# Optimization experiments

Measured on AMD Instinct MI355X. Metric: run time of the kernel, lower is better.

The kernel has to match this reference:

```python
import jax, jax.numpy as jnp
import numpy as np

K = 4096          # num_embeddings
D = 256           # embedding_dim
COMMIT = 0.25     # commitment_cost


def setup_inputs() -> dict:
    key = jax.random.key(0)
    k1, k2 = jax.random.split(key)
    z = jax.random.normal(k1, (16, D, 32, 32), dtype=jnp.float32)
    # codebook init: uniform(-1/K, 1/K) as in the torch module
    emb = jax.random.uniform(k2, (K, D), dtype=jnp.float32,
                             minval=-1.0 / K, maxval=1.0 / K)
    return {"z": z, "emb": emb}


def reference(z, emb):
    B, Dm, H, W = z.shape
    # (B, D, H, W) -> (B*H*W, D)
    z_flat = jnp.transpose(z, (0, 2, 3, 1)).reshape(-1, Dm)
    # squared L2 distances to every codebook vector: (N, K)
    distances = (jnp.sum(z_flat * z_flat, axis=1, keepdims=True)
                 + jnp.sum(emb * emb, axis=1)
                 - 2.0 * jnp.matmul(z_flat, emb.T))
    encoding_indices = jnp.argmin(distances, axis=1)            # (N,)
    encodings = jax.nn.one_hot(encoding_indices, emb.shape[0],
                               dtype=z.dtype)                   # (N, K)
    quantized = jnp.take(emb, encoding_indices, axis=0)         # == encodings @ emb

    sg = jax.lax.stop_gradient
    e_latent_loss = jnp.mean((sg(quantized) - z_flat) ** 2)
    q_latent_loss = jnp.mean((quantized - sg(z_flat)) ** 2)
    loss = q_latent_loss + COMMIT * e_latent_loss

    avg_probs = jnp.mean(encodings, axis=0)
    perplexity = jnp.exp(-jnp.sum(avg_probs * jnp.log(avg_probs + 1e-10)))

    # straight-through estimator
    quantized = z_flat + sg(quantized - z_flat)
    # NOTE: faithful to source: torch does .view(B, D, H, W) on the (N, D)
    # flat tensor WITHOUT permuting back -- a plain reshape, replicated here.
    quantized = quantized.reshape(B, Dm, H, W)
    return quantized, loss, perplexity, encodings
```

## Files before the change

### kernel.cpp

```cpp
#include <hip/hip_runtime.h>

#define NN 16384
#define KK 4096
#define DD 256

typedef __attribute__((ext_vector_type(8))) short short8;
typedef __attribute__((ext_vector_type(4))) float f32x4;

static __device__ __forceinline__ unsigned short f2bf(float f) {
  unsigned u = __float_as_uint(f);
  return (unsigned short)((u + 0x7FFFu + ((u >> 16) & 1u)) >> 16);
}

static __device__ __forceinline__ unsigned int mono(float f) {
  unsigned u = __float_as_uint(f);
  return (u & 0x80000000u) ? ~u : (u | 0x80000000u);
}

__global__ __launch_bounds__(256) void vq_prep(
    const float* __restrict__ z, const float* __restrict__ emb,
    unsigned short* __restrict__ zb, unsigned short* __restrict__ eb,
    float* __restrict__ e2g, unsigned long long* __restrict__ keys,
    unsigned int* __restrict__ counts, float* __restrict__ lossacc,
    unsigned int* __restrict__ donecnt) {
  __shared__ unsigned short t[64][72];
  const int tid = threadIdx.x;
  const int bx = blockIdx.x;

  if (bx < 1024) {
    const int b = bx >> 6, rem = bx & 63, dt = rem >> 4, ht = rem & 15;
    const float* src = z + (long)b * 262144 + (long)dt * 65536 + ht * 64;
    #pragma unroll
    for (int p = 0; p < 16; ++p) {
      int idx = p * 256 + tid;
      int dl = idx >> 6, hl = idx & 63;
      t[hl][dl] = f2bf(src[dl * 1024 + hl]);
    }
    __syncthreads();
    unsigned short* dst = zb + ((long)b * 1024 + (long)ht * 64) * DD + dt * 64;
    #pragma unroll
    for (int p = 0; p < 2; ++p) {
      int idx = p * 256 + tid;
      int hl = idx >> 3, c8 = idx & 7;
      short8 v = *reinterpret_cast<const short8*>(&t[hl][c8 * 8]);
      *reinterpret_cast<short8*>(&dst[(long)hl * DD + c8 * 8]) = v;
    }
  } else if (bx < 2048) {
    const int wid = tid >> 6, lane = tid & 63;
    const int row = (bx - 1024) * 4 + wid;
    float4 v = *reinterpret_cast<const float4*>(&emb[row * DD + lane * 4]);
    ushort4 w;
    w.x = f2bf(v.x); w.y = f2bf(v.y); w.z = f2bf(v.z); w.w = f2bf(v.w);
    *reinterpret_cast<ushort4*>(&eb[row * DD + lane * 4]) = w;
    float s = v.x * v.x + v.y * v.y + v.z * v.z + v.w * v.w;
    #pragma unroll
    for (int o = 1; o < 64; o <<= 1) s += __shfl_xor(s, o);
    if (lane == 0) e2g[row] = s;
  } else {
    int tt = (bx - 2048) * 256 + tid;
    #pragma unroll
    for (int i = 0; i < 8; ++i) keys[tt * 8 + i] = ~0ull;
    counts[tt * 2] = 0u;
    counts[tt * 2 + 1] = 0u;
    if (tt == 0) { lossacc[0] = 0.f; donecnt[0] = 0u; }
  }
}

__global__ __launch_bounds__(256) void vq_gemm(
    const unsigned short* __restrict__ eb, const unsigned short* __restrict__ zb,
    const float* __restrict__ e2g, unsigned long long* __restrict__ keys,
    float* __restrict__ enc) {
  __shared__ unsigned short At[2][128 * 64];
  __shared__ unsigned short Bt[2][128 * 64];
  __shared__ float e2s[128];
  __shared__ unsigned long long wkey[2][128];

  const int tid = threadIdx.x;
  const int bm = blockIdx.x;
  const int bn = blockIdx.y;
  const int lane = tid & 63, wid = tid >> 6;
  const int wm = wid >> 1, wn = wid & 1;
  const int l16 = lane & 15, g4 = lane >> 4;

  if (tid < 128) {
    e2s[tid] = e2g[bm * 128 + tid];
    wkey[0][tid] = ~0ull;
    wkey[1][tid] = ~0ull;
  }

  const long abase = (long)bm * 128 * DD;
  const long bbase = (long)bn * 128 * DD;
  const int lr = lane >> 3, lc = (lane & 7) * 8;

  auto stage = [&](int buf, int kt) {
    #pragma unroll
    for (int c = 0; c < 4; ++c) {
      const int row0 = wid * 32 + c * 8;
      const unsigned short* ga =
          eb + abase + (long)(row0 + lr) * DD + kt * 64 + lc;
      __builtin_amdgcn_global_load_lds(
          (const __attribute__((address_space(1))) void*)ga,
          (__attribute__((address_space(3))) void*)&At[buf][row0 * 64], 16, 0, 0);
      const unsigned short* gb =
          zb + bbase + (long)(row0 + lr) * DD + kt * 64 + lc;
      __builtin_amdgcn_global_load_lds(
          (const __attribute__((address_space(1))) void*)gb,
          (__attribute__((address_space(3))) void*)&Bt[buf][row0 * 64], 16, 0, 0);
    }
  };

  f32x4 acc[4][4];
  #pragma unroll
  for (int mi = 0; mi < 4; ++mi)
    #pragma unroll
    for (int ni = 0; ni < 4; ++ni) acc[mi][ni] = (f32x4){0.f, 0.f, 0.f, 0.f};

  stage(0, 0);
  #pragma unroll
  for (int kt = 0; kt < 4; ++kt) {
    const int cur = kt & 1;
    asm volatile("s_waitcnt lgkmcnt(0)" ::: "memory");
    __builtin_amdgcn_s_barrier();
    if (kt < 3) {
      stage(cur ^ 1, kt + 1);
      asm volatile("s_waitcnt vmcnt(8)" ::: "memory");
    } else {
      asm volatile("s_waitcnt vmcnt(0)" ::: "memory");
    }
    __builtin_amdgcn_s_barrier();

    #pragma unroll
    for (int kk = 0; kk < 2; ++kk) {
      short8 a[4], b[4];
      #pragma unroll
      for (int mi = 0; mi < 4; ++mi)
        a[mi] = *reinterpret_cast<const short8*>(
            &At[cur][(wm * 64 + mi * 16 + l16) * 64 + kk * 32 + g4 * 8]);
      #pragma unroll
      for (int ni = 0; ni < 4; ++ni)
        b[ni] = *reinterpret_cast<const short8*>(
            &Bt[cur][(wn * 64 + ni * 16 + l16) * 64 + kk * 32 + g4 * 8]);
      #pragma unroll
      for (int mi = 0; mi < 4; ++mi)
        #pragma unroll
        for (int ni = 0; ni < 4; ++ni)
          acc[mi][ni] = __builtin_amdgcn_mfma_f32_16x16x32_bf16(
              a[mi], b[ni], acc[mi][ni], 0, 0, 0);
    }
  }

  #pragma unroll
  for (int ni = 0; ni < 4; ++ni) {
    float bv = INFINITY;
    int bi = 0;
    #pragma unroll
    for (int mi = 0; mi < 4; ++mi) {
      #pragma unroll
      for (int r = 0; r < 4; ++r) {
        int krow = wm * 64 + mi * 16 + g4 * 4 + r;
        float s = fmaf(-2.0f, acc[mi][ni][r], e2s[krow]);
        if (s < bv) { bv = s; bi = bm * 128 + krow; }
      }
    }
    unsigned long long key =
        ((unsigned long long)mono(bv) << 32) | (unsigned)bi;
    unsigned long long o;
    o = __shfl_xor(key, 16); if (o < key) key = o;
    o = __shfl_xor(key, 32); if (o < key) key = o;
    if (g4 == 0) wkey[wm][wn * 64 + ni * 16 + l16] = key;
  }
  __syncthreads();
  if (tid < 128) {
    unsigned long long k0 = wkey[0][tid], k1 = wkey[1][tid];
    atomicMin(&keys[(long)bn * 128 + tid], k0 < k1 ? k0 : k1);
  }

  {
    const long base = ((long)(bm * 128 + bn)) * 16384;
    const f32x4 zero4 = (f32x4){0.f, 0.f, 0.f, 0.f};
    #pragma unroll
    for (int i = 0; i < 16; ++i)
      *reinterpret_cast<f32x4*>(&enc[base + (long)(i * 256 + tid) * 4]) = zero4;
  }
}

__global__ __launch_bounds__(256) void vq_finish(
    const float* __restrict__ z, const float* __restrict__ emb,
    const unsigned long long* __restrict__ keys, unsigned int* __restrict__ counts,
    float* __restrict__ lossacc, unsigned int* __restrict__ donecnt,
    float* __restrict__ outq, float* __restrict__ enc, float* __restrict__ outs) {
  __shared__ float ztile[64][257];
  __shared__ int sidx[64];
  __shared__ float wsum[4];
  __shared__ double sh[256];
  __shared__ unsigned int lastflag;

  const int tid = threadIdx.x;
  const int n0 = blockIdx.x * 64;
  const long zbase = (long)(n0 >> 10) * 262144 + (long)(n0 & 1023);

  {
    int n4 = (tid & 15) << 2;
    int dl = tid >> 4;
    for (int p = 0; p < 16; ++p) {
      int d = p * 16 + dl;
      float4 v = *reinterpret_cast<const float4*>(&z[zbase + (long)d * 1024 + n4]);
      ztile[n4 + 0][d] = v.x;
      ztile[n4 + 1][d] = v.y;
      ztile[n4 + 2][d] = v.z;
      ztile[n4 + 3][d] = v.w;
    }
  }
  if (tid < 64) {
    int n = n0 + tid;
    int idx = (int)(keys[n] & 0xFFFFFFFFULL);
    sidx[tid] = idx;
    atomicAdd(&counts[idx], 1u);
    enc[(long)n * KK + idx] = 1.0f;
  }
  __syncthreads();

  float lacc = 0.f;
  const int d = tid;
  #pragma unroll 4
  for (int nl = 0; nl < 64; ++nl) {
    int idx = sidx[nl];
    float e = emb[idx * DD + d];
    float zz = ztile[nl][d];
    float df = e - zz;
    lacc += df * df;
    outq[(long)(n0 + nl) * DD + d] = zz + (e - zz);
  }
  #pragma unroll
  for (int o = 1; o < 64; o <<= 1) lacc += __shfl_xor(lacc, o);
  if ((tid & 63) == 0) wsum[tid >> 6] = lacc;
  __syncthreads();
  if (tid == 0) atomicAdd(lossacc, wsum[0] + wsum[1] + wsum[2] + wsum[3]);

  __threadfence();
  if (tid == 0) lastflag = (atomicAdd(donecnt, 1u) == (unsigned)(NN / 64 - 1));
  __syncthreads();
  if (lastflag) {
    double ent = 0.0;
    for (int k = tid; k < KK; k += 256) {
      unsigned c = atomicAdd(&counts[k], 0u);
      double p = (double)c / (double)NN;
      ent += p * log(p + 1e-10);
    }
    sh[tid] = ent;
    __syncthreads();
    for (int s = 128; s > 0; s >>= 1) {
      if (tid < s) sh[tid] += sh[tid + s];
      __syncthreads();
    }
    if (tid == 0) {
      float la = atomicAdd(lossacc, 0.f);
      outs[0] = la * 1.25f / ((float)NN * (float)DD);
      outs[1] = (float)exp(-sh[0]);
    }
  }
}

extern "C" void kernel_launch(void* const* d_in, const int* in_sizes, int n_in,
                              void* d_out, int out_size, void* d_ws, size_t ws_size,
                              hipStream_t stream) {
  const float* z = (const float*)d_in[0];
  const float* emb = (const float*)d_in[1];
  float* out = (float*)d_out;
  float* outq = out;
  float* outs = out + 4194304;
  float* enc = out + 4194306;

  char* ws = (char*)d_ws;
  unsigned short* zb = (unsigned short*)ws;
  unsigned short* eb = (unsigned short*)(ws + 8388608);
  float* e2g = (float*)(ws + 10485760);
  unsigned long long* keys = (unsigned long long*)(ws + 10502144);
  unsigned int* counts = (unsigned int*)(ws + 10633216);
  float* lossacc = (float*)(ws + 10649600);
  unsigned int* donecnt = (unsigned int*)(ws + 10649604);

  vq_prep<<<2056, 256, 0, stream>>>(z, emb, zb, eb, e2g, keys, counts,
                                    lossacc, donecnt);
  vq_gemm<<<dim3(32, 128), 256, 0, stream>>>(eb, zb, e2g, keys, enc);
  vq_finish<<<NN / 64, 256, 0, stream>>>(z, emb, keys, counts, lossacc,
                                         donecnt, outq, enc, outs);
}
```

Baseline: 382.2 us.

## Remap GEMM workgroups per XCD and drop LDS double buffering

Switches the GEMM grid from 2D to a 1D launch and remaps block IDs so that each XCD (chiplet) handles a contiguous group of 16 z-row tiles while iterating over codebook tiles, which is meant to improve L2 reuse of the z tiles within a chiplet. It also replaces the double-buffered async LDS pipeline with a single buffer loaded between two __syncthreads. This halves LDS use, which may allow higher occupancy, but global loads no longer overlap with MFMA work inside a block.

```diff
diff --git a/kernel.cpp b/kernel.cpp
--- a/kernel.cpp
+++ b/kernel.cpp
@@ -70,14 +70,16 @@
     const unsigned short* __restrict__ eb, const unsigned short* __restrict__ zb,
     const float* __restrict__ e2g, unsigned long long* __restrict__ keys,
     float* __restrict__ enc) {
-  __shared__ unsigned short At[2][128 * 64];
-  __shared__ unsigned short Bt[2][128 * 64];
+  __shared__ unsigned short At[128 * 64];
+  __shared__ unsigned short Bt[128 * 64];
   __shared__ float e2s[128];
   __shared__ unsigned long long wkey[2][128];
 
   const int tid = threadIdx.x;
-  const int bm = blockIdx.x;
-  const int bn = blockIdx.y;
+  const int wgid = blockIdx.x;
+  const int xcd = wgid & 7, slot = wgid >> 3;
+  const int bn = xcd * 16 + (slot & 15);
+  const int bm = slot >> 4;
   const int lane = tid & 63, wid = tid >> 6;
   const int wm = wid >> 1, wn = wid & 1;
   const int l16 = lane & 15, g4 = lane >> 4;
@@ -90,24 +92,6 @@
 
   const long abase = (long)bm * 128 * DD;
   const long bbase = (long)bn * 128 * DD;
-  const int lr = lane >> 3, lc = (lane & 7) * 8;
-
-  auto stage = [&](int buf, int kt) {
-    #pragma unroll
-    for (int c = 0; c < 4; ++c) {
-      const int row0 = wid * 32 + c * 8;
-      const unsigned short* ga =
-          eb + abase + (long)(row0 + lr) * DD + kt * 64 + lc;
-      __builtin_amdgcn_global_load_lds(
-          (const __attribute__((address_space(1))) void*)ga,
-          (__attribute__((address_space(3))) void*)&At[buf][row0 * 64], 16, 0, 0);
-      const unsigned short* gb =
-          zb + bbase + (long)(row0 + lr) * DD + kt * 64 + lc;
-      __builtin_amdgcn_global_load_lds(
-          (const __attribute__((address_space(1))) void*)gb,
-          (__attribute__((address_space(3))) void*)&Bt[buf][row0 * 64], 16, 0, 0);
-    }
-  };
 
   f32x4 acc[4][4];
   #pragma unroll
@@ -115,19 +99,26 @@
     #pragma unroll
     for (int ni = 0; ni < 4; ++ni) acc[mi][ni] = (f32x4){0.f, 0.f, 0.f, 0.f};
 
-  stage(0, 0);
-  #pragma unroll
   for (int kt = 0; kt < 4; ++kt) {
-    const int cur = kt & 1;
-    asm volatile("s_waitcnt lgkmcnt(0)" ::: "memory");
-    __builtin_amdgcn_s_barrier();
-    if (kt < 3) {
-      stage(cur ^ 1, kt + 1);
-      asm volatile("s_waitcnt vmcnt(8)" ::: "memory");
-    } else {
-      asm volatile("s_waitcnt vmcnt(0)" ::: "memory");
-    }
-    __builtin_amdgcn_s_barrier();
+    __syncthreads();
+    {
+      const int lr = lane >> 3, lc = (lane & 7) * 8;
+      #pragma unroll
+      for (int c = 0; c < 4; ++c) {
+        const int row0 = wid * 32 + c * 8;
+        const unsigned short* ga =
+            eb + abase + (long)(row0 + lr) * DD + kt * 64 + lc;
+        __builtin_amdgcn_global_load_lds(
+            (const __attribute__((address_space(1))) void*)ga,
+            (__attribute__((address_space(3))) void*)&At[row0 * 64], 16, 0, 0);
+        const unsigned short* gb =
+            zb + bbase + (long)(row0 + lr) * DD + kt * 64 + lc;
+        __builtin_amdgcn_global_load_lds(
+            (const __attribute__((address_space(1))) void*)gb,
+            (__attribute__((address_space(3))) void*)&Bt[row0 * 64], 16, 0, 0);
+      }
+    }
+    __syncthreads();
 
     #pragma unroll
     for (int kk = 0; kk < 2; ++kk) {
@@ -135,11 +126,11 @@
       #pragma unroll
       for (int mi = 0; mi < 4; ++mi)
         a[mi] = *reinterpret_cast<const short8*>(
-            &At[cur][(wm * 64 + mi * 16 + l16) * 64 + kk * 32 + g4 * 8]);
+            &At[(wm * 64 + mi * 16 + l16) * 64 + kk * 32 + g4 * 8]);
       #pragma unroll
       for (int ni = 0; ni < 4; ++ni)
         b[ni] = *reinterpret_cast<const short8*>(
-            &Bt[cur][(wn * 64 + ni * 16 + l16) * 64 + kk * 32 + g4 * 8]);
+            &Bt[(wn * 64 + ni * 16 + l16) * 64 + kk * 32 + g4 * 8]);
       #pragma unroll
       for (int mi = 0; mi < 4; ++mi)
         #pragma unroll
@@ -282,7 +273,7 @@
 
   vq_prep<<<2056, 256, 0, stream>>>(z, emb, zb, eb, e2g, keys, counts,
                                     lossacc, donecnt);
-  vq_gemm<<<dim3(32, 128), 256, 0, stream>>>(eb, zb, e2g, keys, enc);
+  vq_gemm<<<4096, 256, 0, stream>>>(eb, zb, e2g, keys, enc);
   vq_finish<<<NN / 64, 256, 0, stream>>>(z, emb, keys, counts, lossacc,
                                          donecnt, outq, enc, outs);
 }
```

Measured after the change: 380.8 us. About the same (-0.4%).
